# Kernel tuning notes

Measured on AMD Instinct MI355X. Metric: run time of the kernel, lower is better.

## Reference

```python
import jax, jax.numpy as jnp
import numpy as np

N_NODES = 50000


def gcn_conv(x, W, b, src, dst):
    # PyG GCNConv: h = x @ W; add self-loops; norm = deg^{-1/2}[src]*deg^{-1/2}[dst];
    # out = scatter_add(norm * h[src] -> dst) + bias
    h = x @ W  # [N, out]
    ones = jnp.ones(src.shape[0], dtype=x.dtype)
    deg = jax.ops.segment_sum(ones, dst, num_segments=N_NODES) + 1.0  # +1 for self-loop
    inv_sqrt = deg ** -0.5
    norm = inv_sqrt[src] * inv_sqrt[dst]  # [E]
    msgs = h[src] * norm[:, None]  # [E, out]
    agg = jax.ops.segment_sum(msgs, dst, num_segments=N_NODES)
    # self-loop contribution: norm_ii = deg_i^{-1}
    agg = agg + h * (inv_sqrt * inv_sqrt)[:, None]
    return agg + b


def setup_inputs() -> dict:
    key = jax.random.key(0)
    k1, k2, k3, k4 = jax.random.split(key, 4)
    d_in, d_h = 256, 256
    x = jax.random.normal(k1, (N_NODES, d_in), dtype=jnp.float32)
    edge_index = jax.random.randint(k2, (2, 800000), 0, N_NODES, dtype=jnp.int64)
    # Glorot-style params (GCNConv linear has no bias; separate bias added post-agg)
    W1 = jax.random.normal(k3, (d_in, d_h), dtype=jnp.float32) / np.sqrt(d_in)
    W2 = jax.random.normal(k4, (d_h, d_h), dtype=jnp.float32) / np.sqrt(d_h)
    b1 = jnp.zeros((d_h,), dtype=jnp.float32)
    b2 = jnp.zeros((d_h,), dtype=jnp.float32)
    return {"x": x, "edge_index": edge_index, "W1": W1, "b1": b1, "W2": W2, "b2": b2}


def reference(x, edge_index, W1, b1, W2, b2):
    src, dst = edge_index[0], edge_index[1]
    h = jax.nn.relu(gcn_conv(x, W1, b1, src, dst))
    h = jax.nn.relu(gcn_conv(h, W2, b2, src, dst))
    # global_mean_pool with batch=arange(N) assigns each node its own graph -> identity
    return h
```

## Files before the change

### kernel.cpp

```cpp
#include <hip/hip_runtime.h>
#include <hip/hip_bf16.h>

typedef unsigned short u16;
typedef unsigned int u32;

#define N_NODES 50000
#define N_EDGES 800000
#define DHID 256
#define ELLW 64

typedef __attribute__((ext_vector_type(8))) _Float16 f16x8;
typedef __attribute__((ext_vector_type(4))) float f32x4;
typedef __attribute__((ext_vector_type(2))) float f32x2;

__device__ __forceinline__ u16 f2bf(float f) {
    u32 u = __float_as_uint(f);
    u32 r = (u + 0x7FFFu + ((u >> 16) & 1u)) >> 16;
    return (u16)r;
}
__device__ __forceinline__ u16 f2h(float f) {
    _Float16 h = (_Float16)f;
    union { _Float16 h; u16 u; } c; c.h = h;
    return c.u;
}

__global__ void zero_kernel(int* __restrict__ deg, u32* __restrict__ hs32) {
    int j = blockIdx.x * 256 + threadIdx.x;
    if (j < N_NODES) deg[j] = 0;
    if (j < 128) hs32[(size_t)N_NODES * 128 + j] = 0;
}

#define SPLIT_BLKS 12500
#define W_BLKS 512
__global__ void prep_kernel(const float* __restrict__ x, u16* __restrict__ xf,
                            const float* __restrict__ W1, const float* __restrict__ W2,
                            u16* __restrict__ W1t, u16* __restrict__ W2t) {
    const int b = blockIdx.x, tid = threadIdx.x;
    if (b < SPLIT_BLKS) {
        int i = b * 256 + tid;
        float4 v = ((const float4*)x)[i];
        u16 h0 = f2h(v.x), h1 = f2h(v.y), h2 = f2h(v.z), h3 = f2h(v.w);
        uint2 hv;
        hv.x = (u32)h0 | ((u32)h1 << 16);
        hv.y = (u32)h2 | ((u32)h3 << 16);
        ((uint2*)xf)[i] = hv;
    } else {
        int idx = b - SPLIT_BLKS;
        int y = idx >> 8, n = idx & 255, k = tid;
        const float* W = y ? W2 : W1;
        u16* o = y ? W2t : W1t;
        o[n * 256 + k] = f2h(W[k * 256 + n]);
    }
}

#define FILL_BLKS 782
__global__ void fill_kernel(const int* __restrict__ src, const int* __restrict__ dst,
                            int* __restrict__ deg, u16* __restrict__ col16) {
    const int tid = threadIdx.x;
    const int e0 = blockIdx.x * 1024 + tid;
    int ds[4], ps[4], ss[4];
    bool ok[4];
#pragma unroll
    for (int q = 0; q < 4; ++q) {
        int e = e0 + q * 256;
        ok[q] = (e < N_EDGES);
        if (ok[q]) { ds[q] = dst[e]; ss[q] = src[e]; }
    }
#pragma unroll
    for (int q = 0; q < 4; ++q)
        if (ok[q]) ps[q] = atomicAdd(&deg[ds[q]], 1);
#pragma unroll
    for (int q = 0; q < 4; ++q)
        if (ok[q] && ps[q] < ELLW) col16[(size_t)ds[q] * ELLW + ps[q]] = (u16)ss[q];
}

__global__ __launch_bounds__(256, 2) void gemm_f16_kernel(
    const u16* __restrict__ Af, const u16* __restrict__ Bt,
    const int* __restrict__ deg, u16* __restrict__ out, int M) {
    const int tid = threadIdx.x;
    const int wave = tid >> 6;
    const int lane = tid & 63;
    const int quad = lane >> 4, l16 = lane & 15;
    const int rowbase = blockIdx.x * 256 + wave * 64;
    const int n0 = blockIdx.y * 128;

    f32x4 acc[4][8] = {};

    size_t aoff[4];
#pragma unroll
    for (int rt = 0; rt < 4; ++rt) {
        int ar = rowbase + rt * 16 + l16;
        if (ar >= M) ar = M - 1;
        aoff[rt] = (size_t)ar * 256 + quad * 8;
    }
    size_t boff[8];
#pragma unroll
    for (int nt = 0; nt < 8; ++nt)
        boff[nt] = (size_t)(n0 + nt * 16 + l16) * 256 + quad * 8;

    for (int kt = 0; kt < 8; ++kt) {
        const int ko = kt * 32;
        f16x8 bfr[8], afr[4];
#pragma unroll
        for (int nt = 0; nt < 8; ++nt)
            bfr[nt] = *(const f16x8*)&Bt[boff[nt] + ko];
#pragma unroll
        for (int rt = 0; rt < 4; ++rt)
            afr[rt] = *(const f16x8*)&Af[aoff[rt] + ko];
#pragma unroll
        for (int rt = 0; rt < 4; ++rt)
#pragma unroll
            for (int nt = 0; nt < 8; ++nt)
                acc[rt][nt] = __builtin_amdgcn_mfma_f32_16x16x32_f16(afr[rt], bfr[nt], acc[rt][nt], 0, 0, 0);
    }

#pragma unroll
    for (int rt = 0; rt < 4; ++rt) {
#pragma unroll
        for (int r = 0; r < 4; ++r) {
            int row = rowbase + rt * 16 + quad * 4 + r;
            if (row < M) {
                float s = rsqrtf((float)deg[row] + 1.0f);
#pragma unroll
                for (int nt = 0; nt < 8; ++nt) {
                    int c = n0 + nt * 16 + l16;
                    out[(size_t)row * 256 + c] = f2bf(acc[rt][nt][r] * s);
                }
            }
        }
    }
}

__global__ __launch_bounds__(256) void agg_kernel(
    const u16* __restrict__ hs, const u16* __restrict__ col16,
    const int* __restrict__ deg, const float* __restrict__ bias,
    u16* __restrict__ out_f16, float* __restrict__ out_f,
    int mode, int Nn) {
    const int wave = threadIdx.x >> 6, lane = threadIdx.x & 63;
    const int i = blockIdx.x * 4 + wave;
    if (i >= Nn) return;

    const int cnt = deg[i];
    const size_t ebase = (size_t)i * ELLW;
    int entry = Nn;
    if (lane == 0) entry = i;
    else if (lane - 1 < cnt) entry = (int)col16[ebase + lane - 1];
    int entries = cnt + 1;
    if (entries > 64) entries = 64;
    const int nb = (entries + 3) >> 2;
    const size_t lofs = (size_t)lane * 4;

    f32x2 a01 = {0.f, 0.f}, a23 = {0.f, 0.f};

#define ISSUE(b, x0, x1, x2, x3)                                                \
    {                                                                           \
        int e0 = __builtin_amdgcn_readlane(entry, (b) * 4 + 0);                 \
        int e1 = __builtin_amdgcn_readlane(entry, (b) * 4 + 1);                 \
        int e2 = __builtin_amdgcn_readlane(entry, (b) * 4 + 2);                 \
        int e3 = __builtin_amdgcn_readlane(entry, (b) * 4 + 3);                 \
        x0 = *(const uint2*)(hs + (size_t)e0 * 256 + lofs);                     \
        x1 = *(const uint2*)(hs + (size_t)e1 * 256 + lofs);                     \
        x2 = *(const uint2*)(hs + (size_t)e2 * 256 + lofs);                     \
        x3 = *(const uint2*)(hs + (size_t)e3 * 256 + lofs);                     \
    }
#define ACCUM(v)                                                                \
    {                                                                           \
        f32x2 p0, p1;                                                           \
        p0.x = __uint_as_float(v.x << 16);                                      \
        p0.y = __uint_as_float(v.x & 0xffff0000u);                              \
        p1.x = __uint_as_float(v.y << 16);                                      \
        p1.y = __uint_as_float(v.y & 0xffff0000u);                              \
        a01 += p0; a23 += p1;                                                   \
    }

    uint2 c0, c1, c2, c3, d0, d1, d2, d3, n0v, n1v, n2v, n3v;
    ISSUE(0, c0, c1, c2, c3);
    if (nb > 1) ISSUE(1, d0, d1, d2, d3);
    for (int b = 0; b < nb; ++b) {
        const bool more2 = (b + 2 < nb);
        if (more2) ISSUE(b + 2, n0v, n1v, n2v, n3v);
        ACCUM(c0); ACCUM(c1); ACCUM(c2); ACCUM(c3);
        c0 = d0; c1 = d1; c2 = d2; c3 = d3;
        d0 = n0v; d1 = n1v; d2 = n2v; d3 = n3v;
    }
    {
        int cap = cnt < ELLW ? cnt : ELLW;
        for (int j = 63; j < cap; ++j) {
            int s = (int)col16[ebase + j];
            uint2 v = *(const uint2*)(hs + (size_t)s * 256 + lofs);
            ACCUM(v);
        }
    }
#undef ISSUE
#undef ACCUM

    const float inv = rsqrtf((float)cnt + 1.0f);
    float4 bb = *(const float4*)(bias + lane * 4);
    float r0 = fmaxf(fmaf(a01.x, inv, bb.x), 0.0f);
    float r1 = fmaxf(fmaf(a01.y, inv, bb.y), 0.0f);
    float r2 = fmaxf(fmaf(a23.x, inv, bb.z), 0.0f);
    float r3 = fmaxf(fmaf(a23.y, inv, bb.w), 0.0f);
    const size_t o = (size_t)i * 256 + lane * 4;
    if (mode == 0) {
        u16 h0 = f2h(r0), h1 = f2h(r1), h2 = f2h(r2), h3 = f2h(r3);
        uint2 w;
        w.x = (u32)h0 | ((u32)h1 << 16);
        w.y = (u32)h2 | ((u32)h3 << 16);
        *(uint2*)(out_f16 + o) = w;
    } else {
        *(float4*)(out_f + o) = make_float4(r0, r1, r2, r3);
    }
}

extern "C" void kernel_launch(void* const* d_in, const int* in_sizes, int n_in,
                              void* d_out, int out_size, void* d_ws, size_t ws_size,
                              hipStream_t stream) {
    const float* x = (const float*)d_in[0];
    const int* ei = (const int*)d_in[1];
    const float* W1 = (const float*)d_in[2];
    const float* b1 = (const float*)d_in[3];
    const float* W2 = (const float*)d_in[4];
    const float* b2 = (const float*)d_in[5];
    float* out = (float*)d_out;

    const int Nn = N_NODES, E = N_EDGES;
    const int* srcp = ei;
    const int* dstp = ei + E;

    char* p = (char*)d_ws;
    auto take = [&](size_t bytes) -> void* {
        void* r = (void*)p;
        p += (bytes + 255) & ~(size_t)255;
        return r;
    };
    u16* hs    = (u16*)take((size_t)(Nn + 1) * DHID * 2);
    u16* col16 = (u16*)take((size_t)Nn * ELLW * 2);
    int* deg   = (int*)take((size_t)Nn * 4);
    u16* W1t   = (u16*)take(256 * 256 * 2);
    u16* W2t   = (u16*)take(256 * 256 * 2);
    size_t used = (size_t)(p - (char*)d_ws);
    size_t af_bytes = (size_t)Nn * DHID * 2;
    u16* Af = (ws_size >= used + af_bytes) ? (u16*)take(af_bytes) : (u16*)d_out;

    zero_kernel<<<196, 256, 0, stream>>>(deg, (u32*)hs);
    prep_kernel<<<SPLIT_BLKS + W_BLKS, 256, 0, stream>>>(x, Af, W1, W2, W1t, W2t);
    fill_kernel<<<FILL_BLKS, 256, 0, stream>>>(srcp, dstp, deg, col16);

    const int gm = (Nn + 255) / 256;
    gemm_f16_kernel<<<dim3(gm, 2), 256, 0, stream>>>(Af, W1t, deg, hs, Nn);
    agg_kernel<<<(Nn + 3) / 4, 256, 0, stream>>>(hs, col16, deg, b1, Af, nullptr, 0, Nn);
    gemm_f16_kernel<<<dim3(gm, 2), 256, 0, stream>>>(Af, W2t, deg, hs, Nn);
    agg_kernel<<<(Nn + 3) / 4, 256, 0, stream>>>(hs, col16, deg, b2, nullptr, out, 1, Nn);
}
```

Before: 331.0 us.

## Fuse x fp16 conversion into first GEMM and add LDS-tiled second GEMM

Result: faster. 314.1 us (-5.1%).

```diff
diff --git a/kernel.cpp b/kernel.cpp
--- a/kernel.cpp
+++ b/kernel.cpp
@@ -23,29 +23,22 @@
     union { _Float16 h; u16 u; } c; c.h = h;
     return c.u;
 }
-
-__global__ void zero_kernel(int* __restrict__ deg, u32* __restrict__ hs32) {
-    int j = blockIdx.x * 256 + threadIdx.x;
-    if (j < N_NODES) deg[j] = 0;
-    if (j < 128) hs32[(size_t)N_NODES * 128 + j] = 0;
-}
-
-#define SPLIT_BLKS 12500
-#define W_BLKS 512
-__global__ void prep_kernel(const float* __restrict__ x, u16* __restrict__ xf,
-                            const float* __restrict__ W1, const float* __restrict__ W2,
-                            u16* __restrict__ W1t, u16* __restrict__ W2t) {
+__device__ __forceinline__ void gl_lds16(const void* g, void* l) {
+    __builtin_amdgcn_global_load_lds(
+        (const __attribute__((address_space(1))) u32*)g,
+        (__attribute__((address_space(3))) u32*)l, 16, 0, 0);
+}
+
+__global__ void zero_w_kernel(int* __restrict__ deg, u32* __restrict__ hs32,
+                              const float* __restrict__ W1, const float* __restrict__ W2,
+                              u16* __restrict__ W1t, u16* __restrict__ W2t) {
     const int b = blockIdx.x, tid = threadIdx.x;
-    if (b < SPLIT_BLKS) {
-        int i = b * 256 + tid;
-        float4 v = ((const float4*)x)[i];
-        u16 h0 = f2h(v.x), h1 = f2h(v.y), h2 = f2h(v.z), h3 = f2h(v.w);
-        uint2 hv;
-        hv.x = (u32)h0 | ((u32)h1 << 16);
-        hv.y = (u32)h2 | ((u32)h3 << 16);
-        ((uint2*)xf)[i] = hv;
+    if (b < 196) {
+        int j = b * 256 + tid;
+        if (j < N_NODES) deg[j] = 0;
+        if (j < 128) hs32[(size_t)N_NODES * 128 + j] = 0;
     } else {
-        int idx = b - SPLIT_BLKS;
+        int idx = b - 196;
         int y = idx >> 8, n = idx & 255, k = tid;
         const float* W = y ? W2 : W1;
         u16* o = y ? W2t : W1t;
@@ -53,29 +46,29 @@
     }
 }
 
-#define FILL_BLKS 782
+#define FILL_BLKS 391
 __global__ void fill_kernel(const int* __restrict__ src, const int* __restrict__ dst,
                             int* __restrict__ deg, u16* __restrict__ col16) {
     const int tid = threadIdx.x;
-    const int e0 = blockIdx.x * 1024 + tid;
-    int ds[4], ps[4], ss[4];
-    bool ok[4];
-#pragma unroll
-    for (int q = 0; q < 4; ++q) {
+    const int e0 = blockIdx.x * 2048 + tid;
+    int ds[8], ps[8], ss[8];
+    bool ok[8];
+#pragma unroll
+    for (int q = 0; q < 8; ++q) {
         int e = e0 + q * 256;
         ok[q] = (e < N_EDGES);
         if (ok[q]) { ds[q] = dst[e]; ss[q] = src[e]; }
     }
 #pragma unroll
-    for (int q = 0; q < 4; ++q)
+    for (int q = 0; q < 8; ++q)
         if (ok[q]) ps[q] = atomicAdd(&deg[ds[q]], 1);
 #pragma unroll
-    for (int q = 0; q < 4; ++q)
+    for (int q = 0; q < 8; ++q)
         if (ok[q] && ps[q] < ELLW) col16[(size_t)ds[q] * ELLW + ps[q]] = (u16)ss[q];
 }
 
-__global__ __launch_bounds__(256, 2) void gemm_f16_kernel(
-    const u16* __restrict__ Af, const u16* __restrict__ Bt,
+__global__ __launch_bounds__(256, 2) void gemm_f32a_kernel(
+    const float* __restrict__ Ax, const u16* __restrict__ Bt,
     const int* __restrict__ deg, u16* __restrict__ out, int M) {
     const int tid = threadIdx.x;
     const int wave = tid >> 6;
@@ -105,8 +98,16 @@
         for (int nt = 0; nt < 8; ++nt)
             bfr[nt] = *(const f16x8*)&Bt[boff[nt] + ko];
 #pragma unroll
-        for (int rt = 0; rt < 4; ++rt)
-            afr[rt] = *(const f16x8*)&Af[aoff[rt] + ko];
+        for (int rt = 0; rt < 4; ++rt) {
+            float4 u = *(const float4*)&Ax[aoff[rt] + ko];
+            float4 v = *(const float4*)&Ax[aoff[rt] + ko + 4];
+            f16x8 a;
+            a[0] = (_Float16)u.x; a[1] = (_Float16)u.y;
+            a[2] = (_Float16)u.z; a[3] = (_Float16)u.w;
+            a[4] = (_Float16)v.x; a[5] = (_Float16)v.y;
+            a[6] = (_Float16)v.z; a[7] = (_Float16)v.w;
+            afr[rt] = a;
+        }
 #pragma unroll
         for (int rt = 0; rt < 4; ++rt)
 #pragma unroll
@@ -125,6 +126,73 @@
                 for (int nt = 0; nt < 8; ++nt) {
                     int c = n0 + nt * 16 + l16;
                     out[(size_t)row * 256 + c] = f2bf(acc[rt][nt][r] * s);
+                }
+            }
+        }
+    }
+}
+
+__global__ __launch_bounds__(256) void gemm_f16_kernel(
+    const u16* __restrict__ Af, const u16* __restrict__ Bt,
+    const int* __restrict__ deg, u16* __restrict__ out, int M) {
+    __shared__ u16 As[128 * 32];
+    __shared__ u16 Bs[128 * 32];
+    const int tid = threadIdx.x;
+    const int wave = tid >> 6;
+    const int lane = tid & 63;
+    const int wm = wave >> 1, wn = wave & 1;
+    const int quad = lane >> 4, l16 = lane & 15;
+    const int m0 = blockIdx.x * 128;
+    const int n0 = blockIdx.y * 128;
+
+    f32x4 acc[4][4] = {};
+
+    const int row0 = tid >> 2, row1 = (256 + tid) >> 2;
+    const int kk = (tid & 3) * 8;
+    int ar0 = m0 + row0; if (ar0 >= M) ar0 = M - 1;
+    int ar1 = m0 + row1; if (ar1 >= M) ar1 = M - 1;
+    const size_t aoff0 = (size_t)ar0 * 256 + kk;
+    const size_t aoff1 = (size_t)ar1 * 256 + kk;
+    const size_t boff0 = (size_t)(n0 + row0) * 256 + kk;
+    const size_t boff1 = (size_t)(n0 + row1) * 256 + kk;
+    const size_t l0 = (size_t)(wave * 64) * 8;
+    const size_t l1 = (size_t)(256 + wave * 64) * 8;
+
+    for (int ko = 0; ko < 8; ++ko) {
+        const int koff = ko * 32;
+        __syncthreads();
+        gl_lds16(Af + aoff0 + koff, &As[l0]);
+        gl_lds16(Af + aoff1 + koff, &As[l1]);
+        gl_lds16(Bt + boff0 + koff, &Bs[l0]);
+        gl_lds16(Bt + boff1 + koff, &Bs[l1]);
+        asm volatile("s_waitcnt vmcnt(0)" ::: "memory");
+        __syncthreads();
+
+        f16x8 af[4], bf[4];
+#pragma unroll
+        for (int mi = 0; mi < 4; ++mi)
+            af[mi] = *(const f16x8*)&As[(wm * 64 + mi * 16 + l16) * 32 + quad * 8];
+#pragma unroll
+        for (int ni = 0; ni < 4; ++ni)
+            bf[ni] = *(const f16x8*)&Bs[(wn * 64 + ni * 16 + l16) * 32 + quad * 8];
+#pragma unroll
+        for (int mi = 0; mi < 4; ++mi)
+#pragma unroll
+            for (int ni = 0; ni < 4; ++ni)
+                acc[mi][ni] = __builtin_amdgcn_mfma_f32_16x16x32_f16(af[mi], bf[ni], acc[mi][ni], 0, 0, 0);
+    }
+
+#pragma unroll
+    for (int mi = 0; mi < 4; ++mi) {
+#pragma unroll
+        for (int r = 0; r < 4; ++r) {
+            int row = m0 + wm * 64 + mi * 16 + quad * 4 + r;
+            if (row < M) {
+                float s = rsqrtf((float)deg[row] + 1.0f);
+#pragma unroll
+                for (int ni = 0; ni < 4; ++ni) {
+                    int c = n0 + wn * 64 + ni * 16 + l16;
+                    out[(size_t)row * 256 + c] = f2bf(acc[mi][ni][r] * s);
                 }
             }
         }
@@ -242,13 +310,11 @@
     size_t af_bytes = (size_t)Nn * DHID * 2;
     u16* Af = (ws_size >= used + af_bytes) ? (u16*)take(af_bytes) : (u16*)d_out;
 
-    zero_kernel<<<196, 256, 0, stream>>>(deg, (u32*)hs);
-    prep_kernel<<<SPLIT_BLKS + W_BLKS, 256, 0, stream>>>(x, Af, W1, W2, W1t, W2t);
+    zero_w_kernel<<<708, 256, 0, stream>>>(deg, (u32*)hs, W1, W2, W1t, W2t);
     fill_kernel<<<FILL_BLKS, 256, 0, stream>>>(srcp, dstp, deg, col16);
 
-    const int gm = (Nn + 255) / 256;
-    gemm_f16_kernel<<<dim3(gm, 2), 256, 0, stream>>>(Af, W1t, deg, hs, Nn);
+    gemm_f32a_kernel<<<dim3((Nn + 255) / 256, 2), 256, 0, stream>>>(x, W1t, deg, hs, Nn);
     agg_kernel<<<(Nn + 3) / 4, 256, 0, stream>>>(hs, col16, deg, b1, Af, nullptr, 0, Nn);
-    gemm_f16_kernel<<<dim3(gm, 2), 256, 0, stream>>>(Af, W2t, deg, hs, Nn);
+    gemm_f16_kernel<<<dim3((Nn + 127) / 128, 2), 256, 0, stream>>>(Af, W2t, deg, hs, Nn);
     agg_kernel<<<(Nn + 3) / 4, 256, 0, stream>>>(hs, col16, deg, b2, nullptr, out, 1, Nn);
 }
```
